# Kernel optimization log

Measured on AMD Instinct MI355X. Metric: run time of the kernel, lower is better.

The kernel has to match this reference:

```python
import jax, jax.numpy as jnp
import numpy as np

N_NODES = 50000
N_EDGES = 800000
DIM = 96
N_LAYERS = 3
N_GRAPHS = 128
OUT_DIM = 10


def setup_inputs() -> dict:
    key = jax.random.key(0)
    ks = jax.random.split(key, 9)
    s = 1.0 / np.sqrt(DIM)
    return {
        "x": jax.random.normal(ks[0], (N_NODES, DIM), dtype=jnp.float32),
        "edge_index": jax.random.randint(ks[1], (2, N_EDGES), 0, N_NODES, dtype=jnp.int32),
        "batch": jnp.sort(jax.random.randint(ks[2], (N_NODES,), 0, N_GRAPHS, dtype=jnp.int32)),
        "W1": jax.random.normal(ks[3], (N_LAYERS, DIM, DIM), dtype=jnp.float32) * s,
        "W2": jax.random.normal(ks[4], (N_LAYERS, DIM, DIM), dtype=jnp.float32) * s,
        "cw1": jax.random.normal(ks[5], (DIM, DIM), dtype=jnp.float32) * s,
        "cb1": jax.random.normal(ks[6], (DIM,), dtype=jnp.float32) * s,
        "cw2": jax.random.normal(ks[7], (DIM, OUT_DIM), dtype=jnp.float32) * s,
        "cb2": jax.random.normal(ks[8], (OUT_DIM,), dtype=jnp.float32) * s,
    }


def reference(x, edge_index, batch, W1, W2, cw1, cb1, cw2, cb2):
    src, dst = edge_index[0], edge_index[1]
    h = x
    for l in range(N_LAYERS):
        self_part = h @ W1[l]                       # [N, D]
        # transform at node level then gather per edge (same math as per-edge W2(x_j))
        msg = (h @ W2[l])[src]                      # [E, D]
        neighbor_part = jax.ops.segment_sum(msg, dst, num_segments=N_NODES)
        h = jax.nn.relu(self_part + neighbor_part)
    graph_emb = jax.ops.segment_sum(h, batch, num_segments=N_GRAPHS)  # [G, D]
    hidden = jax.nn.relu(graph_emb @ cw1 + cb1)
    return hidden @ cw2 + cb2                       # [G, OUT_DIM]
```

## Files before the change

kernel.cpp:

```cpp
#include <hip/hip_runtime.h>

#define N_NODES   50000
#define N_EDGES   800000
#define DIM       96
#define N_GRAPHS  128
#define OUT_DIM   10
#define NPAD      50048
#define ZROW      N_NODES
#define NBINS     391
#define P1_BLOCKS 128
#define EPB       (N_EDGES / P1_BLOCKS)
#define SLICECAP  48
#define CAP       64
#define LPAD      104

#define CAST_NB   ((N_NODES * 12 + 255) / 256)
#define CONV_NB   ((3 * DIM * 2 * DIM + 255) / 256)

typedef __attribute__((ext_vector_type(8))) short          short8;
typedef __attribute__((ext_vector_type(8))) unsigned short u16x8;
typedef __attribute__((ext_vector_type(4))) float          f32x4;

__device__ __forceinline__ float b2f(unsigned short u) {
    union { unsigned int i; float f; } v; v.i = ((unsigned int)u) << 16; return v.f;
}
__device__ __forceinline__ unsigned short f2b(float f) {
    union { float f; unsigned int i; } v; v.f = f;
    unsigned int u = v.i;
    return (unsigned short)((u + 0x7fffu + ((u >> 16) & 1u)) >> 16);
}

__global__ __launch_bounds__(256) void prep_pass1(
    const float* __restrict__ x,  const float* __restrict__ W1,
    const float* __restrict__ W2, const int* __restrict__ src,
    const int* __restrict__ dst,  unsigned short* __restrict__ harr,
    unsigned short* __restrict__ harrB,
    unsigned short* __restrict__ Bt, int* __restrict__ binned,
    int* __restrict__ cnt)
{
    __shared__ int cur[NBINS];
    const int b = blockIdx.x;
    const int t = threadIdx.x;

    if (b < P1_BLOCKS) {
        const int e0 = b * EPB;
        for (int i = t; i < NBINS; i += 256) cur[i] = 0;
        __syncthreads();
        for (int e = e0 + t; e < e0 + EPB; e += 256) {
            const int d   = dst[e];
            const int bin = d >> 7;
            const int pos = atomicAdd(&cur[bin], 1);
            if (pos < SLICECAP)
                binned[((size_t)bin * P1_BLOCKS + b) * SLICECAP + pos]
                    = ((d & 127) << 16) | src[e];
        }
        __syncthreads();
        for (int i = t; i < NBINS; i += 256)
            cnt[i * P1_BLOCKS + b] = min(cur[i], SLICECAP);
    } else if (b < P1_BLOCKS + CAST_NB) {
        const int tid = (b - P1_BLOCKS) * 256 + t;
        if (tid >= N_NODES * 12) return;
        const int node = tid / 12;
        const int c    = (tid - node * 12) * 8;
        const float4 v0 = *(const float4*)(x + (size_t)node * DIM + c);
        const float4 v1 = *(const float4*)(x + (size_t)node * DIM + c + 4);
        u16x8 o;
        o[0] = f2b(v0.x); o[1] = f2b(v0.y); o[2] = f2b(v0.z); o[3] = f2b(v0.w);
        o[4] = f2b(v1.x); o[5] = f2b(v1.y); o[6] = f2b(v1.z); o[7] = f2b(v1.w);
        *(u16x8*)(harr + (size_t)node * DIM + c) = o;
    } else if (b < P1_BLOCKS + CAST_NB + CONV_NB) {
        const int idx = (b - P1_BLOCKS - CAST_NB) * 256 + t;
        if (idx >= 3 * DIM * 2 * DIM) return;
        const int l   = idx / (DIM * 2 * DIM);
        const int rem = idx - l * (DIM * 2 * DIM);
        const int n   = rem / (2 * DIM);
        const int k   = rem - n * (2 * DIM);
        const float v = (k < DIM) ? W1[(size_t)l * DIM * DIM + k * DIM + n]
                                  : W2[(size_t)l * DIM * DIM + (k - DIM) * DIM + n];
        Bt[idx] = f2b(v);
    } else {
        if (t < 24) {
            u16x8 z;
#pragma unroll
            for (int i = 0; i < 8; i++) z[i] = 0;
            unsigned short* p = (t < 12) ? (harr  + (size_t)ZROW * DIM + t * 8)
                                         : (harrB + (size_t)ZROW * DIM + (t - 12) * 8);
            *(u16x8*)p = z;
        }
    }
}

__global__ __launch_bounds__(256) void pass2_scatter(const int* __restrict__ cnt,
                                                     const int* __restrict__ binned,
                                                     int* __restrict__ csrc,
                                                     int* __restrict__ deg)
{
    __shared__ int ncnt[128];
    const int bin = blockIdx.x;
    const int t   = threadIdx.x;
    const int n0  = bin << 7;

    if (t < 128) ncnt[t] = 0;
    __syncthreads();

    const int slice = t >> 1;
    const int par   = t & 1;
    const int c     = cnt[bin * P1_BLOCKS + slice];
    const int* __restrict__ bb = binned + ((size_t)bin * P1_BLOCKS + slice) * SLICECAP;

    for (int i = par; i < c; i += 2) {
        const int v    = bb[i];
        const int dlow = v >> 16;
        const int s    = v & 0xffff;
        const int pos  = atomicAdd(&ncnt[dlow], 1);
        if (pos < CAP) csrc[(size_t)(n0 + dlow) * CAP + pos] = s;
    }
    __syncthreads();

    if (t < 128 && n0 + t < N_NODES) {
        const int dn = min(ncnt[t], CAP);
        const int dp = (dn + 3) & ~3;
        int* __restrict__ bkt = csrc + (size_t)(n0 + t) * CAP;
        for (int p = dn; p < dp; p++) bkt[p] = ZROW;
        deg[n0 + t] = dp;
    }
}

#define LOAD4(x0,x1,x2,x3,y0,y1,y2,y3,base) do {                            \
    const int4 sI = *(const int4*)(bkt + (base));                           \
    const unsigned short* P0 = hb + (size_t)sI.x * DIM;                     \
    const unsigned short* P1 = hb + (size_t)sI.y * DIM;                     \
    const unsigned short* P2 = hb + (size_t)sI.z * DIM;                     \
    const unsigned short* P3 = hb + (size_t)sI.w * DIM;                     \
    x0 = *(const u16x8*)P0; y0 = *(const u16x8*)(P0 + 8);                   \
    x1 = *(const u16x8*)P1; y1 = *(const u16x8*)(P1 + 8);                   \
    x2 = *(const u16x8*)P2; y2 = *(const u16x8*)(P2 + 8);                   \
    x3 = *(const u16x8*)P3; y3 = *(const u16x8*)(P3 + 8);                   \
} while (0)

#define ACC4(x0,x1,x2,x3,y0,y1,y2,y3) do {                                  \
    _Pragma("unroll")                                                       \
    for (int i = 0; i < 8; i++) {                                           \
        a[i]     += (b2f(x0[i]) + b2f(x1[i])) + (b2f(x2[i]) + b2f(x3[i]));  \
        a[i + 8] += (b2f(y0[i]) + b2f(y1[i])) + (b2f(y2[i]) + b2f(y3[i]));  \
    }                                                                       \
} while (0)

__global__ __launch_bounds__(384) void gnn_layer(
    const unsigned short* __restrict__ harr, const int* __restrict__ deg,
    const int* __restrict__ csrc, const unsigned short* __restrict__ Btl,
    unsigned short* __restrict__ hout)
{
    __shared__ unsigned short aggLds[64][LPAD];
    const int t       = threadIdx.x;
    const int rowBase = blockIdx.x * 64;

    const int lane = t & 63;
    const int w    = t >> 6;
    const int m    = lane & 15;
    const int q    = lane >> 4;
    short8 bfrag[6];
#pragma unroll
    for (int s = 0; s < 6; s++)
        bfrag[s] = *(const short8*)(Btl + (size_t)(w * 16 + m) * (2 * DIM) + s * 32 + q * 8);

    {
        const int r    = t / 6;
        const int sub  = t - r * 6;
        const int node = rowBase + r;
        const int off  = sub * 16;

        float a[16];
#pragma unroll
        for (int i = 0; i < 16; i++) a[i] = 0.f;

        if (node < N_NODES) {
            const int nb = deg[node] >> 2;
            const int* __restrict__ bkt = csrc + (size_t)node * CAP;
            const unsigned short* __restrict__ hb = harr + off;

            u16x8 va0, va1, va2, va3, ua0, ua1, ua2, ua3;
            u16x8 wa0, wa1, wa2, wa3, xa0, xa1, xa2, xa3;

            if (nb > 0) {
                LOAD4(va0, va1, va2, va3, ua0, ua1, ua2, ua3, 0);
                int b = 1;
                for (; b + 1 < nb; b += 2) {
                    LOAD4(wa0, wa1, wa2, wa3, xa0, xa1, xa2, xa3, b * 4);
                    ACC4(va0, va1, va2, va3, ua0, ua1, ua2, ua3);
                    LOAD4(va0, va1, va2, va3, ua0, ua1, ua2, ua3, (b + 1) * 4);
                    ACC4(wa0, wa1, wa2, wa3, xa0, xa1, xa2, xa3);
                }
                if (b < nb) {
                    LOAD4(wa0, wa1, wa2, wa3, xa0, xa1, xa2, xa3, b * 4);
                    ACC4(va0, va1, va2, va3, ua0, ua1, ua2, ua3);
                    ACC4(wa0, wa1, wa2, wa3, xa0, xa1, xa2, xa3);
                } else {
                    ACC4(va0, va1, va2, va3, ua0, ua1, ua2, ua3);
                }
            }
        }

        u16x8 o0, o1;
#pragma unroll
        for (int i = 0; i < 8; i++) { o0[i] = f2b(a[i]); o1[i] = f2b(a[i + 8]); }
        *(u16x8*)(&aggLds[r][off])     = o0;
        *(u16x8*)(&aggLds[r][off + 8]) = o1;
    }
    __syncthreads();

    f32x4 accv[4];
#pragma unroll
    for (int r = 0; r < 4; r++) {
        const int rb = rowBase + r * 16;
        f32x4 acc = {0.f, 0.f, 0.f, 0.f};
        const unsigned short* ah = harr + (size_t)(rb + m) * DIM + q * 8;
#pragma unroll
        for (int s = 0; s < 3; s++) {
            const short8 af = *(const short8*)(ah + s * 32);
            acc = __builtin_amdgcn_mfma_f32_16x16x32_bf16(af, bfrag[s], acc, 0, 0, 0);
        }
#pragma unroll
        for (int s = 0; s < 3; s++) {
            const short8 af = *(const short8*)(&aggLds[r * 16 + m][s * 32 + q * 8]);
            acc = __builtin_amdgcn_mfma_f32_16x16x32_bf16(af, bfrag[s + 3], acc, 0, 0, 0);
        }
        accv[r] = acc;
    }
    __syncthreads();

#pragma unroll
    for (int r = 0; r < 4; r++)
#pragma unroll
        for (int i = 0; i < 4; i++)
            aggLds[r * 16 + q * 4 + i][w * 16 + m] = f2b(fmaxf(accv[r][i], 0.f));
    __syncthreads();

#pragma unroll
    for (int k = 0; k < 2; k++) {
        const int idx = t + k * 384;
        const int row = idx / 12;
        const int ch  = idx - row * 12;
        const int grow = rowBase + row;
        if (grow < N_NODES)
            *(u16x8*)(hout + (size_t)grow * DIM + ch * 8)
                = *(const u16x8*)(&aggLds[row][ch * 8]);
    }
}

__global__ __launch_bounds__(960) void pool_classify(
    const unsigned short* __restrict__ h, const int* __restrict__ batch,
    const float* __restrict__ cw1, const float* __restrict__ cb1,
    const float* __restrict__ cw2, const float* __restrict__ cb2,
    float* __restrict__ out)
{
    const int g = blockIdx.x;
    const int t = threadIdx.x;

    int lo = 0, hi = N_NODES;
    while (lo < hi) { int m = (lo + hi) >> 1; if (batch[m] < g) lo = m + 1; else hi = m; }
    const int start = lo;
    hi = N_NODES;
    while (lo < hi) { int m = (lo + hi) >> 1; if (batch[m] < g + 1) lo = m + 1; else hi = m; }
    const int end = lo;

    __shared__ float part[10][DIM];
    __shared__ float gr[DIM];
    __shared__ float hid[DIM];

    const int col = t % DIM;
    const int ty  = t / DIM;

    float s = 0.f;
    for (int n = start + ty; n < end; n += 10)
        s += b2f(h[(size_t)n * DIM + col]);
    part[ty][col] = s;
    __syncthreads();
    if (ty == 0) {
        float acc = 0.f;
#pragma unroll
        for (int p = 0; p < 10; p++) acc += part[p][col];
        gr[col] = acc;
    }
    __syncthreads();

    if (ty < 4) {
        float hsum = 0.f;
        const int k0 = ty * (DIM / 4);
#pragma unroll 4
        for (int k = k0; k < k0 + DIM / 4; k++)
            hsum += gr[k] * cw1[k * DIM + col];
        part[ty][col] = hsum;
    }
    __syncthreads();
    if (ty == 0)
        hid[col] = fmaxf(part[0][col] + part[1][col] + part[2][col] + part[3][col]
                         + cb1[col], 0.f);
    __syncthreads();

    if (t < OUT_DIM) {
        float o = cb2[t];
#pragma unroll 4
        for (int k = 0; k < DIM; k++) o += hid[k] * cw2[k * OUT_DIM + t];
        out[g * OUT_DIM + t] = o;
    }
}

extern "C" void kernel_launch(void* const* d_in, const int* in_sizes, int n_in,
                              void* d_out, int out_size, void* d_ws, size_t ws_size,
                              hipStream_t stream)
{
    const float* x     = (const float*)d_in[0];
    const int*   ei    = (const int*)  d_in[1];
    const int*   batch = (const int*)  d_in[2];
    const float* W1    = (const float*)d_in[3];
    const float* W2    = (const float*)d_in[4];
    const float* cw1   = (const float*)d_in[5];
    const float* cb1   = (const float*)d_in[6];
    const float* cw2   = (const float*)d_in[7];
    const float* cb2   = (const float*)d_in[8];
    float*       out   = (float*)d_out;

    const int* src = ei;
    const int* dst = ei + N_EDGES;

    unsigned short* bufA = (unsigned short*)d_ws;
    unsigned short* bufB = bufA + (size_t)NPAD * DIM;
    unsigned short* Bt   = bufB + (size_t)NPAD * DIM;
    int*   cnt    = (int*)(Bt + 3 * DIM * 2 * DIM);
    int*   binned = cnt + NBINS * P1_BLOCKS;
    int*   csrc   = binned + (size_t)NBINS * P1_BLOCKS * SLICECAP;
    int*   deg    = csrc + (size_t)N_NODES * CAP;

    prep_pass1<<<P1_BLOCKS + CAST_NB + CONV_NB + 1, 256, 0, stream>>>(
        x, W1, W2, src, dst, bufA, bufB, Bt, binned, cnt);
    pass2_scatter<<<NBINS, 256, 0, stream>>>(cnt, binned, csrc, deg);

    unsigned short* hin  = bufA;
    unsigned short* hout = bufB;
    for (int l = 0; l < 3; l++) {
        gnn_layer<<<NPAD / 64, 384, 0, stream>>>(hin, deg, csrc,
                                                 Bt + (size_t)l * DIM * 2 * DIM, hout);
        unsigned short* tmp = hin; hin = hout; hout = tmp;
    }

    pool_classify<<<N_GRAPHS, 960, 0, stream>>>(hin, batch, cw1, cb1, cw2, cb2, out);
}
```

Before: 261.6 us.

## Gather neighbor features as custom 8-bit floats instead of bf16

Adds a second copy of node features in a custom FP8-like format (E4M3-style, scaled by 0.25) written by the cast kernel and by each layer's epilogue. The neighbor aggregation gathers these 1-byte values, halving the bytes moved per edge in the dominant random-gather phase, and decodes them to fp32 before summing. The cost is extra encode work and an extra store per layer, plus a large loss of precision in the neighbor sum that may break tolerance.

```diff
diff --git a/kernel.cpp b/kernel.cpp
--- a/kernel.cpp
+++ b/kernel.cpp
@@ -30,11 +30,29 @@
     return (unsigned short)((u + 0x7fffu + ((u >> 16) & 1u)) >> 16);
 }
 
+__device__ __forceinline__ unsigned int e8(float f) {
+    union { float f; unsigned int i; } v; v.f = f * 0.25f;
+    const unsigned int u = v.i;
+    const unsigned int s = (u >> 24) & 0x80u;
+    const unsigned int r = (u & 0x7fffffffu) + 0x0007ffffu + ((u >> 20) & 1u);
+    const int ee = (int)(r >> 23) - 120;
+    if (ee < 1)  return s;
+    if (ee > 15) return s | 0x7fu;
+    return s | ((unsigned int)ee << 3) | ((r >> 20) & 7u);
+}
+__device__ __forceinline__ float d8(unsigned int b) {
+    const unsigned int t = b & 0x7fu;
+    union { unsigned int i; float f; } v;
+    v.i = (t < 8u) ? 0u : (((b & 0x80u) << 24) | ((t + 976u) << 20));
+    return v.f;
+}
+
 __global__ __launch_bounds__(256) void prep_pass1(
     const float* __restrict__ x,  const float* __restrict__ W1,
     const float* __restrict__ W2, const int* __restrict__ src,
     const int* __restrict__ dst,  unsigned short* __restrict__ harr,
     unsigned short* __restrict__ harrB,
+    unsigned char* __restrict__ shA, unsigned char* __restrict__ shB,
     unsigned short* __restrict__ Bt, int* __restrict__ binned,
     int* __restrict__ cnt)
 {
@@ -68,6 +86,10 @@
         o[0] = f2b(v0.x); o[1] = f2b(v0.y); o[2] = f2b(v0.z); o[3] = f2b(v0.w);
         o[4] = f2b(v1.x); o[5] = f2b(v1.y); o[6] = f2b(v1.z); o[7] = f2b(v1.w);
         *(u16x8*)(harr + (size_t)node * DIM + c) = o;
+        uint2 ob;
+        ob.x = e8(v0.x) | (e8(v0.y) << 8) | (e8(v0.z) << 16) | (e8(v0.w) << 24);
+        ob.y = e8(v1.x) | (e8(v1.y) << 8) | (e8(v1.z) << 16) | (e8(v1.w) << 24);
+        *(uint2*)(shA + (size_t)node * 96 + c) = ob;
     } else if (b < P1_BLOCKS + CAST_NB + CONV_NB) {
         const int idx = (b - P1_BLOCKS - CAST_NB) * 256 + t;
         if (idx >= 3 * DIM * 2 * DIM) return;
@@ -86,6 +108,12 @@
             unsigned short* p = (t < 12) ? (harr  + (size_t)ZROW * DIM + t * 8)
                                          : (harrB + (size_t)ZROW * DIM + (t - 12) * 8);
             *(u16x8*)p = z;
+        } else if (t < 48) {
+            const int i = t - 24;
+            uint2 z; z.x = 0u; z.y = 0u;
+            unsigned char* p = (i < 12) ? (shA + (size_t)ZROW * 96 + i * 8)
+                                        : (shB + (size_t)ZROW * 96 + (i - 12) * 8);
+            *(uint2*)p = z;
         }
     }
 }
@@ -126,30 +154,29 @@
     }
 }
 
-#define LOAD4(x0,x1,x2,x3,y0,y1,y2,y3,base) do {                            \
+#define LOAD4(x0,x1,x2,x3,base) do {                                        \
     const int4 sI = *(const int4*)(bkt + (base));                           \
-    const unsigned short* P0 = hb + (size_t)sI.x * DIM;                     \
-    const unsigned short* P1 = hb + (size_t)sI.y * DIM;                     \
-    const unsigned short* P2 = hb + (size_t)sI.z * DIM;                     \
-    const unsigned short* P3 = hb + (size_t)sI.w * DIM;                     \
-    x0 = *(const u16x8*)P0; y0 = *(const u16x8*)(P0 + 8);                   \
-    x1 = *(const u16x8*)P1; y1 = *(const u16x8*)(P1 + 8);                   \
-    x2 = *(const u16x8*)P2; y2 = *(const u16x8*)(P2 + 8);                   \
-    x3 = *(const u16x8*)P3; y3 = *(const u16x8*)(P3 + 8);                   \
+    x0 = *(const u16x8*)(hb + (size_t)sI.x * 96);                           \
+    x1 = *(const u16x8*)(hb + (size_t)sI.y * 96);                           \
+    x2 = *(const u16x8*)(hb + (size_t)sI.z * 96);                           \
+    x3 = *(const u16x8*)(hb + (size_t)sI.w * 96);                           \
 } while (0)
 
-#define ACC4(x0,x1,x2,x3,y0,y1,y2,y3) do {                                  \
+#define ACC1(vv) do {                                                       \
     _Pragma("unroll")                                                       \
     for (int i = 0; i < 8; i++) {                                           \
-        a[i]     += (b2f(x0[i]) + b2f(x1[i])) + (b2f(x2[i]) + b2f(x3[i]));  \
-        a[i + 8] += (b2f(y0[i]) + b2f(y1[i])) + (b2f(y2[i]) + b2f(y3[i]));  \
+        const unsigned int u = (unsigned int)(unsigned short)vv[i];         \
+        a[2 * i]     += d8(u & 0xffu);                                      \
+        a[2 * i + 1] += d8(u >> 8);                                         \
     }                                                                       \
 } while (0)
+#define ACC4(x0,x1,x2,x3) do { ACC1(x0); ACC1(x1); ACC1(x2); ACC1(x3); } while (0)
 
 __global__ __launch_bounds__(384) void gnn_layer(
     const unsigned short* __restrict__ harr, const int* __restrict__ deg,
     const int* __restrict__ csrc, const unsigned short* __restrict__ Btl,
-    unsigned short* __restrict__ hout)
+    unsigned short* __restrict__ hout,
+    const unsigned char* __restrict__ shIn, unsigned char* __restrict__ shOut)
 {
     __shared__ unsigned short aggLds[64][LPAD];
     const int t       = threadIdx.x;
@@ -159,6 +186,7 @@
     const int w    = t >> 6;
     const int m    = lane & 15;
     const int q    = lane >> 4;
+
     short8 bfrag[6];
 #pragma unroll
     for (int s = 0; s < 6; s++)
@@ -177,26 +205,26 @@
         if (node < N_NODES) {
             const int nb = deg[node] >> 2;
             const int* __restrict__ bkt = csrc + (size_t)node * CAP;
-            const unsigned short* __restrict__ hb = harr + off;
-
-            u16x8 va0, va1, va2, va3, ua0, ua1, ua2, ua3;
-            u16x8 wa0, wa1, wa2, wa3, xa0, xa1, xa2, xa3;
+            const unsigned char* __restrict__ hb = shIn + off;
+
+            u16x8 va0, va1, va2, va3;
+            u16x8 wa0, wa1, wa2, wa3;
 
             if (nb > 0) {
-                LOAD4(va0, va1, va2, va3, ua0, ua1, ua2, ua3, 0);
+                LOAD4(va0, va1, va2, va3, 0);
                 int b = 1;
                 for (; b + 1 < nb; b += 2) {
-                    LOAD4(wa0, wa1, wa2, wa3, xa0, xa1, xa2, xa3, b * 4);
-                    ACC4(va0, va1, va2, va3, ua0, ua1, ua2, ua3);
-                    LOAD4(va0, va1, va2, va3, ua0, ua1, ua2, ua3, (b + 1) * 4);
-                    ACC4(wa0, wa1, wa2, wa3, xa0, xa1, xa2, xa3);
+                    LOAD4(wa0, wa1, wa2, wa3, b * 4);
+                    ACC4(va0, va1, va2, va3);
+                    LOAD4(va0, va1, va2, va3, (b + 1) * 4);
+                    ACC4(wa0, wa1, wa2, wa3);
                 }
                 if (b < nb) {
-                    LOAD4(wa0, wa1, wa2, wa3, xa0, xa1, xa2, xa3, b * 4);
-                    ACC4(va0, va1, va2, va3, ua0, ua1, ua2, ua3);
-                    ACC4(wa0, wa1, wa2, wa3, xa0, xa1, xa2, xa3);
+                    LOAD4(wa0, wa1, wa2, wa3, b * 4);
+                    ACC4(va0, va1, va2, va3);
+                    ACC4(wa0, wa1, wa2, wa3);
                 } else {
-                    ACC4(va0, va1, va2, va3, ua0, ua1, ua2, ua3);
+                    ACC4(va0, va1, va2, va3);
                 }
             }
         }
@@ -245,6 +273,23 @@
         if (grow < N_NODES)
             *(u16x8*)(hout + (size_t)grow * DIM + ch * 8)
                 = *(const u16x8*)(&aggLds[row][ch * 8]);
+    }
+    {
+        const int row  = t / 6;
+        const int ch   = t - row * 6;
+        const int grow = rowBase + row;
+        if (grow < N_NODES) {
+            const u16x8 h0 = *(const u16x8*)(&aggLds[row][ch * 16]);
+            const u16x8 h1 = *(const u16x8*)(&aggLds[row][ch * 16 + 8]);
+            u16x8 ob;
+#pragma unroll
+            for (int i = 0; i < 4; i++)
+                ob[i] = (unsigned short)(e8(b2f(h0[2 * i])) | (e8(b2f(h0[2 * i + 1])) << 8));
+#pragma unroll
+            for (int i = 0; i < 4; i++)
+                ob[4 + i] = (unsigned short)(e8(b2f(h1[2 * i])) | (e8(b2f(h1[2 * i + 1])) << 8));
+            *(u16x8*)(shOut + (size_t)grow * 96 + ch * 16) = ob;
+        }
     }
 }
 
@@ -331,17 +376,23 @@
     int*   binned = cnt + NBINS * P1_BLOCKS;
     int*   csrc   = binned + (size_t)NBINS * P1_BLOCKS * SLICECAP;
     int*   deg    = csrc + (size_t)N_NODES * CAP;
+    unsigned char* shA = (unsigned char*)(deg + N_NODES);
+    unsigned char* shB = shA + (size_t)(N_NODES + 1) * 96;
 
     prep_pass1<<<P1_BLOCKS + CAST_NB + CONV_NB + 1, 256, 0, stream>>>(
-        x, W1, W2, src, dst, bufA, bufB, Bt, binned, cnt);
+        x, W1, W2, src, dst, bufA, bufB, shA, shB, Bt, binned, cnt);
     pass2_scatter<<<NBINS, 256, 0, stream>>>(cnt, binned, csrc, deg);
 
     unsigned short* hin  = bufA;
     unsigned short* hout = bufB;
+    unsigned char*  shin = shA;
+    unsigned char*  shout = shB;
     for (int l = 0; l < 3; l++) {
         gnn_layer<<<NPAD / 64, 384, 0, stream>>>(hin, deg, csrc,
-                                                 Bt + (size_t)l * DIM * 2 * DIM, hout);
+                                                 Bt + (size_t)l * DIM * 2 * DIM,
+                                                 hout, shin, shout);
         unsigned short* tmp = hin; hin = hout; hout = tmp;
+        unsigned char*  tms = shin; shin = shout; shout = tms;
     }
 
     pool_classify<<<N_GRAPHS, 960, 0, stream>>>(hin, batch, cw1, cb1, cw2, cb2, out);
```

Result: slower. 392.1 us (+49.9%).
